# Kernel tuning notes

Hardware: AMD Instinct MI355X
Metric: run time of the kernel (lower is better)

Reference implementation:

```python
import jax, jax.numpy as jnp
import numpy as np

FAST_DECAY = 0.95
FAST_LR = 0.05
SLOW_DECAY = 0.99
SLOW_LR = 0.01
HOMEO_TARGET = 5.0

N = 4096  # batch tokens
D_IN = 4096
D_OUT = 4096


def setup_inputs() -> dict:
    key = jax.random.key(0)
    k1, k2, k3, k4 = jax.random.split(key, 4)
    return {
        "x": jax.random.normal(k1, (N, D_IN), dtype=jnp.float32),
        "weight": jax.random.normal(k2, (D_OUT, D_IN), dtype=jnp.float32) * 0.02,
        "fast_trace": jax.random.normal(k3, (D_OUT, D_IN), dtype=jnp.float32) * 0.001,
        "slow_trace": jax.random.normal(k4, (D_OUT, D_IN), dtype=jnp.float32) * 0.001,
    }


def bitnet_quantize(w):
    # per-row 1.58-bit quantization to {-1,0,1} * scale
    scale = jnp.clip(jnp.mean(jnp.abs(w), axis=1, keepdims=True), 1e-5, None)
    w_q = jnp.clip(jnp.round(w / scale), -1.0, 1.0)
    return w_q * scale


def reference(x, weight, fast_trace, slow_trace):
    w_static = bitnet_quantize(weight)
    w_effective = w_static + 0.1 * fast_trace + 0.05 * slow_trace
    y = x @ w_effective.T  # [N, D_OUT]

    # trace update (torch does this under no_grad)
    y_active = jax.nn.relu(y)
    delta = (y_active.T @ x) / jnp.asarray(x.shape[0], x.dtype)  # [D_OUT, D_IN]
    new_fast = FAST_DECAY * fast_trace + FAST_LR * delta
    fast_norm = jnp.linalg.norm(new_fast)
    new_fast = jnp.where(fast_norm > HOMEO_TARGET,
                         new_fast * (HOMEO_TARGET / (fast_norm + 1e-6)),
                         new_fast)
    new_slow = SLOW_DECAY * slow_trace + SLOW_LR * new_fast
    return y, new_fast, new_slow
```

## Files before the change

kernel.cpp:

```cpp
#include <hip/hip_runtime.h>

#define NTOK 4096
#define DIN  4096
#define DOUT 4096

typedef short bf16x8 __attribute__((ext_vector_type(8)));
typedef float f32x4  __attribute__((ext_vector_type(4)));

__device__ __forceinline__ unsigned short f2bf(float f) {
    union { float f; unsigned u; } v; v.f = f;
    unsigned r = v.u + 0x7FFFu + ((v.u >> 16) & 1u);
    return (unsigned short)(r >> 16);
}

__global__ void scale_kernel(const float* __restrict__ w, double* __restrict__ scale) {
    int row = blockIdx.x;
    const float4* wr = (const float4*)(w + (size_t)row * DIN);
    double s = 0.0;
    for (int i = threadIdx.x; i < DIN / 4; i += 256) {
        float4 v = wr[i];
        s += (double)fabsf(v.x) + (double)fabsf(v.y) + (double)fabsf(v.z) + (double)fabsf(v.w);
    }
    for (int o = 32; o > 0; o >>= 1) s += __shfl_down(s, o);
    __shared__ double part[4];
    int wave = threadIdx.x >> 6, lane = threadIdx.x & 63;
    if (lane == 0) part[wave] = s;
    __syncthreads();
    if (threadIdx.x == 0) {
        double m = (part[0] + part[1] + part[2] + part[3]) * (1.0 / DIN);
        scale[row] = fmax(m, 1e-5);
    }
}

__global__ void weff_kernel(const float* __restrict__ w, const float* __restrict__ fast,
                            const float* __restrict__ slow, const double* __restrict__ scale,
                            unsigned short* __restrict__ weff) {
    int i4 = blockIdx.x * 256 + threadIdx.x;
    double sc = scale[i4 >> 10];
    float4 wv = ((const float4*)w)[i4];
    float4 fv = ((const float4*)fast)[i4];
    float4 sv = ((const float4*)slow)[i4];
    ushort4 o;
    o.x = f2bf((float)(fmin(fmax(rint((double)wv.x / sc), -1.0), 1.0) * sc + 0.1 * (double)fv.x + 0.05 * (double)sv.x));
    o.y = f2bf((float)(fmin(fmax(rint((double)wv.y / sc), -1.0), 1.0) * sc + 0.1 * (double)fv.y + 0.05 * (double)sv.y));
    o.z = f2bf((float)(fmin(fmax(rint((double)wv.z / sc), -1.0), 1.0) * sc + 0.1 * (double)fv.z + 0.05 * (double)sv.z));
    o.w = f2bf((float)(fmin(fmax(rint((double)wv.w / sc), -1.0), 1.0) * sc + 0.1 * (double)fv.w + 0.05 * (double)sv.w));
    ((ushort4*)weff)[i4] = o;
}

__global__ void transpose_kernel(const float* __restrict__ x, unsigned short* __restrict__ xT) {
    __shared__ unsigned short tile[32][33];
    int bi = blockIdx.y, bj = blockIdx.x;
    int tx = threadIdx.x, ty = threadIdx.y;
    #pragma unroll
    for (int s = 0; s < 4; ++s)
        tile[ty + s * 8][tx] = f2bf(x[(size_t)(bi * 32 + ty + s * 8) * DIN + bj * 32 + tx]);
    __syncthreads();
    #pragma unroll
    for (int s = 0; s < 4; ++s)
        xT[(size_t)(bj * 32 + ty + s * 8) * NTOK + bi * 32 + tx] = tile[tx][ty + s * 8];
}

__launch_bounds__(256)
__global__ void gemm1_kernel(const float* __restrict__ x, const unsigned short* __restrict__ weff,
                             float* __restrict__ y, unsigned short* __restrict__ yactT) {
    __shared__ unsigned short smem[16640];
    unsigned short* sA = smem;
    unsigned short* sB = smem + 4096;
    int tid = threadIdx.x;
    int wave = tid >> 6, lane = tid & 63, quad = lane >> 4, l16 = lane & 15;
    int waveRow = wave >> 1, waveCol = wave & 1;
    int rowBase = blockIdx.y * 128;
    int colBase = blockIdx.x * 128;

    f32x4 zero = {0.f, 0.f, 0.f, 0.f};
    f32x4 acc[4][4];
    #pragma unroll
    for (int i = 0; i < 4; ++i)
        #pragma unroll
        for (int j = 0; j < 4; ++j) acc[i][j] = zero;

    for (int k0 = 0; k0 < DIN; k0 += 32) {
        #pragma unroll
        for (int p = 0; p < 4; ++p) {
            int c = tid + p * 256;
            int r = c >> 3, kk = (c & 7) * 4;
            float4 v = *(const float4*)(x + (size_t)(rowBase + r) * DIN + k0 + kk);
            ushort4 o = { f2bf(v.x), f2bf(v.y), f2bf(v.z), f2bf(v.w) };
            *(ushort4*)(sA + r * 32 + kk) = o;
        }
        #pragma unroll
        for (int p = 0; p < 2; ++p) {
            int c = tid + p * 256;
            int r = c >> 2, kk = (c & 3) * 8;
            uint4 v = *(const uint4*)(weff + (size_t)(colBase + r) * DIN + k0 + kk);
            *(uint4*)(sB + r * 32 + kk) = v;
        }
        __syncthreads();
        bf16x8 af[4], bfr[4];
        #pragma unroll
        for (int i = 0; i < 4; ++i)
            af[i] = *(const bf16x8*)(sA + (waveRow * 64 + i * 16 + l16) * 32 + quad * 8);
        #pragma unroll
        for (int j = 0; j < 4; ++j)
            bfr[j] = *(const bf16x8*)(sB + (waveCol * 64 + j * 16 + l16) * 32 + quad * 8);
        #pragma unroll
        for (int i = 0; i < 4; ++i)
            #pragma unroll
            for (int j = 0; j < 4; ++j)
                acc[i][j] = __builtin_amdgcn_mfma_f32_16x16x32_bf16(af[i], bfr[j], acc[i][j], 0, 0, 0);
        __syncthreads();
    }

    #pragma unroll
    for (int i = 0; i < 4; ++i) {
        int rl = waveRow * 64 + i * 16 + quad * 4;
        #pragma unroll
        for (int j = 0; j < 4; ++j) {
            int cl = waveCol * 64 + j * 16 + l16;
            #pragma unroll
            for (int r = 0; r < 4; ++r) {
                float v = acc[i][j][r];
                y[(size_t)(rowBase + rl + r) * DOUT + colBase + cl] = v;
                smem[cl * 130 + rl + r] = f2bf(fmaxf(v, 0.0f));
            }
        }
    }
    __syncthreads();
    int rowT = tid >> 1, cst = (tid & 1) * 64;
    const unsigned int* l32 = (const unsigned int*)smem;
    int b2 = rowT * 65 + (cst >> 1);
    #pragma unroll
    for (int g = 0; g < 8; ++g) {
        uint4 v;
        v.x = l32[b2 + g * 4 + 0]; v.y = l32[b2 + g * 4 + 1];
        v.z = l32[b2 + g * 4 + 2]; v.w = l32[b2 + g * 4 + 3];
        *(uint4*)(yactT + (size_t)(colBase + rowT) * NTOK + rowBase + cst + g * 8) = v;
    }
}

__launch_bounds__(256)
__global__ void gemm2_kernel(const unsigned short* __restrict__ yactT, const unsigned short* __restrict__ xT,
                             const float* __restrict__ fast, float* __restrict__ outFast,
                             float* __restrict__ norm2) {
    __shared__ unsigned short sA[128 * 32];
    __shared__ unsigned short sB[128 * 32];
    __shared__ float redbuf[4];
    int tid = threadIdx.x;
    int wave = tid >> 6, lane = tid & 63, quad = lane >> 4, l16 = lane & 15;
    int waveRow = wave >> 1, waveCol = wave & 1;
    int rowBase = blockIdx.y * 128;
    int colBase = blockIdx.x * 128;

    f32x4 zero = {0.f, 0.f, 0.f, 0.f};
    f32x4 acc[4][4];
    #pragma unroll
    for (int i = 0; i < 4; ++i)
        #pragma unroll
        for (int j = 0; j < 4; ++j) acc[i][j] = zero;

    for (int n0 = 0; n0 < NTOK; n0 += 32) {
        #pragma unroll
        for (int p = 0; p < 2; ++p) {
            int c = tid + p * 256;
            int r = c >> 2, nn = (c & 3) * 8;
            uint4 va = *(const uint4*)(yactT + (size_t)(rowBase + r) * NTOK + n0 + nn);
            *(uint4*)(sA + r * 32 + nn) = va;
            uint4 vb = *(const uint4*)(xT + (size_t)(colBase + r) * NTOK + n0 + nn);
            *(uint4*)(sB + r * 32 + nn) = vb;
        }
        __syncthreads();
        bf16x8 af[4], bfr[4];
        #pragma unroll
        for (int i = 0; i < 4; ++i)
            af[i] = *(const bf16x8*)(sA + (waveRow * 64 + i * 16 + l16) * 32 + quad * 8);
        #pragma unroll
        for (int j = 0; j < 4; ++j)
            bfr[j] = *(const bf16x8*)(sB + (waveCol * 64 + j * 16 + l16) * 32 + quad * 8);
        #pragma unroll
        for (int i = 0; i < 4; ++i)
            #pragma unroll
            for (int j = 0; j < 4; ++j)
                acc[i][j] = __builtin_amdgcn_mfma_f32_16x16x32_bf16(af[i], bfr[j], acc[i][j], 0, 0, 0);
        __syncthreads();
    }

    float lsum = 0.f;
    #pragma unroll
    for (int i = 0; i < 4; ++i) {
        int rg = rowBase + waveRow * 64 + i * 16 + quad * 4;
        #pragma unroll
        for (int j = 0; j < 4; ++j) {
            int cg = colBase + waveCol * 64 + j * 16 + l16;
            #pragma unroll
            for (int r = 0; r < 4; ++r) {
                float d = acc[i][j][r] * (1.0f / 4096.0f);
                float nf = 0.95f * fast[(size_t)(rg + r) * DIN + cg] + 0.05f * d;
                outFast[(size_t)(rg + r) * DIN + cg] = nf;
                lsum += nf * nf;
            }
        }
    }
    for (int o = 32; o > 0; o >>= 1) lsum += __shfl_down(lsum, o);
    if (lane == 0) redbuf[wave] = lsum;
    __syncthreads();
    if (tid == 0) atomicAdd(norm2, redbuf[0] + redbuf[1] + redbuf[2] + redbuf[3]);
}

__global__ void finalize_kernel(const float* __restrict__ slow, float* __restrict__ outFast,
                                float* __restrict__ outSlow, const float* __restrict__ norm2) {
    float n = sqrtf(*norm2);
    float s = (n > 5.0f) ? 5.0f / (n + 1e-6f) : 1.0f;
    int i = blockIdx.x * 256 + threadIdx.x;
    float4 f = ((const float4*)outFast)[i];
    f.x *= s; f.y *= s; f.z *= s; f.w *= s;
    ((float4*)outFast)[i] = f;
    float4 sl = ((const float4*)slow)[i];
    float4 o;
    o.x = 0.99f * sl.x + 0.01f * f.x;
    o.y = 0.99f * sl.y + 0.01f * f.y;
    o.z = 0.99f * sl.z + 0.01f * f.z;
    o.w = 0.99f * sl.w + 0.01f * f.w;
    ((float4*)outSlow)[i] = o;
}

extern "C" void kernel_launch(void* const* d_in, const int* in_sizes, int n_in,
                              void* d_out, int out_size, void* d_ws, size_t ws_size,
                              hipStream_t stream) {
    const float* x    = (const float*)d_in[0];
    const float* w    = (const float*)d_in[1];
    const float* fast = (const float*)d_in[2];
    const float* slow = (const float*)d_in[3];
    float* y       = (float*)d_out;
    float* outFast = y + (size_t)NTOK * DOUT;
    float* outSlow = outFast + (size_t)DOUT * DIN;

    char* ws = (char*)d_ws;
    double* scale = (double*)ws;
    float* norm2  = (float*)(ws + 32768);
    unsigned short* weff  = (unsigned short*)(ws + 32768 + 256);
    unsigned short* xT    = weff + (size_t)DOUT * DIN;
    unsigned short* yactT = xT + (size_t)DIN * NTOK;

    hipMemsetAsync(norm2, 0, sizeof(float), stream);
    scale_kernel<<<4096, 256, 0, stream>>>(w, scale);
    weff_kernel<<<16384, 256, 0, stream>>>(w, fast, slow, scale, weff);
    transpose_kernel<<<dim3(128, 128), dim3(32, 8), 0, stream>>>(x, xT);
    gemm1_kernel<<<dim3(32, 32), 256, 0, stream>>>(x, weff, y, yactT);
    gemm2_kernel<<<dim3(32, 32), 256, 0, stream>>>(yactT, xT, fast, outFast, norm2);
    finalize_kernel<<<16384, 256, 0, stream>>>(slow, outFast, outSlow, norm2);
}
```

Before: 876.2 us.

## Pre-convert x to bf16 and stage GEMM tiles via direct global-to-LDS loads

The transpose kernel now also writes a row-major bf16 copy of x, so gemm1 reads bf16 instead of converting fp32 to bf16 in every tile load. Both GEMMs fill their shared-memory tiles with global_load_lds async copies instead of loading into registers and storing to LDS. This halves gemm1's A-operand traffic and frees VGPRs and instructions. It costs an extra 32MB write in the transpose kernel, and no explicit vmcnt wait before __syncthreads is visible, so LDS visibility depends on the compiler inserting one.

After: 813.9 us. -7.1%, faster.

```diff
diff --git a/kernel.cpp b/kernel.cpp
--- a/kernel.cpp
+++ b/kernel.cpp
@@ -11,6 +11,12 @@
     union { float f; unsigned u; } v; v.f = f;
     unsigned r = v.u + 0x7FFFu + ((v.u >> 16) & 1u);
     return (unsigned short)(r >> 16);
+}
+
+__device__ __forceinline__ void async_copy16(const void* g, void* l) {
+    __builtin_amdgcn_global_load_lds(
+        (const __attribute__((address_space(1))) unsigned int*)g,
+        (__attribute__((address_space(3))) unsigned int*)l, 16, 0, 0);
 }
 
 __global__ void scale_kernel(const float* __restrict__ w, double* __restrict__ scale) {
@@ -48,13 +54,17 @@
     ((ushort4*)weff)[i4] = o;
 }
 
-__global__ void transpose_kernel(const float* __restrict__ x, unsigned short* __restrict__ xT) {
+__global__ void transpose_kernel(const float* __restrict__ x, unsigned short* __restrict__ xbf,
+                                 unsigned short* __restrict__ xT) {
     __shared__ unsigned short tile[32][33];
     int bi = blockIdx.y, bj = blockIdx.x;
     int tx = threadIdx.x, ty = threadIdx.y;
     #pragma unroll
-    for (int s = 0; s < 4; ++s)
-        tile[ty + s * 8][tx] = f2bf(x[(size_t)(bi * 32 + ty + s * 8) * DIN + bj * 32 + tx]);
+    for (int s = 0; s < 4; ++s) {
+        unsigned short b = f2bf(x[(size_t)(bi * 32 + ty + s * 8) * DIN + bj * 32 + tx]);
+        tile[ty + s * 8][tx] = b;
+        xbf[(size_t)(bi * 32 + ty + s * 8) * DIN + bj * 32 + tx] = b;
+    }
     __syncthreads();
     #pragma unroll
     for (int s = 0; s < 4; ++s)
@@ -62,7 +72,7 @@
 }
 
 __launch_bounds__(256)
-__global__ void gemm1_kernel(const float* __restrict__ x, const unsigned short* __restrict__ weff,
+__global__ void gemm1_kernel(const unsigned short* __restrict__ xbf, const unsigned short* __restrict__ weff,
                              float* __restrict__ y, unsigned short* __restrict__ yactT) {
     __shared__ unsigned short smem[16640];
     unsigned short* sA = smem;
@@ -73,6 +83,8 @@
     int rowBase = blockIdx.y * 128;
     int colBase = blockIdx.x * 128;
 
+    int srow = tid >> 2, skk = (tid & 3) * 8;
+
     f32x4 zero = {0.f, 0.f, 0.f, 0.f};
     f32x4 acc[4][4];
     #pragma unroll
@@ -82,19 +94,11 @@
 
     for (int k0 = 0; k0 < DIN; k0 += 32) {
         #pragma unroll
-        for (int p = 0; p < 4; ++p) {
-            int c = tid + p * 256;
-            int r = c >> 3, kk = (c & 7) * 4;
-            float4 v = *(const float4*)(x + (size_t)(rowBase + r) * DIN + k0 + kk);
-            ushort4 o = { f2bf(v.x), f2bf(v.y), f2bf(v.z), f2bf(v.w) };
-            *(ushort4*)(sA + r * 32 + kk) = o;
-        }
-        #pragma unroll
         for (int p = 0; p < 2; ++p) {
-            int c = tid + p * 256;
-            int r = c >> 2, kk = (c & 3) * 8;
-            uint4 v = *(const uint4*)(weff + (size_t)(colBase + r) * DIN + k0 + kk);
-            *(uint4*)(sB + r * 32 + kk) = v;
+            async_copy16(xbf + (size_t)(rowBase + srow + p * 64) * DIN + k0 + skk,
+                         sA + (tid + p * 256) * 8);
+            async_copy16(weff + (size_t)(colBase + srow + p * 64) * DIN + k0 + skk,
+                         sB + (tid + p * 256) * 8);
         }
         __syncthreads();
         bf16x8 af[4], bfr[4];
@@ -152,6 +156,8 @@
     int rowBase = blockIdx.y * 128;
     int colBase = blockIdx.x * 128;
 
+    int srow = tid >> 2, skk = (tid & 3) * 8;
+
     f32x4 zero = {0.f, 0.f, 0.f, 0.f};
     f32x4 acc[4][4];
     #pragma unroll
@@ -162,12 +168,10 @@
     for (int n0 = 0; n0 < NTOK; n0 += 32) {
         #pragma unroll
         for (int p = 0; p < 2; ++p) {
-            int c = tid + p * 256;
-            int r = c >> 2, nn = (c & 3) * 8;
-            uint4 va = *(const uint4*)(yactT + (size_t)(rowBase + r) * NTOK + n0 + nn);
-            *(uint4*)(sA + r * 32 + nn) = va;
-            uint4 vb = *(const uint4*)(xT + (size_t)(colBase + r) * NTOK + n0 + nn);
-            *(uint4*)(sB + r * 32 + nn) = vb;
+            async_copy16(yactT + (size_t)(rowBase + srow + p * 64) * NTOK + n0 + skk,
+                         sA + (tid + p * 256) * 8);
+            async_copy16(xT + (size_t)(colBase + srow + p * 64) * NTOK + n0 + skk,
+                         sB + (tid + p * 256) * 8);
         }
         __syncthreads();
         bf16x8 af[4], bfr[4];
@@ -239,14 +243,15 @@
     double* scale = (double*)ws;
     float* norm2  = (float*)(ws + 32768);
     unsigned short* weff  = (unsigned short*)(ws + 32768 + 256);
-    unsigned short* xT    = weff + (size_t)DOUT * DIN;
+    unsigned short* xbf   = weff + (size_t)DOUT * DIN;
+    unsigned short* xT    = xbf + (size_t)NTOK * DIN;
     unsigned short* yactT = xT + (size_t)DIN * NTOK;
 
     hipMemsetAsync(norm2, 0, sizeof(float), stream);
     scale_kernel<<<4096, 256, 0, stream>>>(w, scale);
     weff_kernel<<<16384, 256, 0, stream>>>(w, fast, slow, scale, weff);
-    transpose_kernel<<<dim3(128, 128), dim3(32, 8), 0, stream>>>(x, xT);
-    gemm1_kernel<<<dim3(32, 32), 256, 0, stream>>>(x, weff, y, yactT);
+    transpose_kernel<<<dim3(128, 128), dim3(32, 8), 0, stream>>>(x, xbf, xT);
+    gemm1_kernel<<<dim3(32, 32), 256, 0, stream>>>(xbf, weff, y, yactT);
     gemm2_kernel<<<dim3(32, 32), 256, 0, stream>>>(yactT, xT, fast, outFast, norm2);
     finalize_kernel<<<16384, 256, 0, stream>>>(slow, outFast, outSlow, norm2);
 }
```
